# Performance work log

Measured on AMD Instinct MI355X. Metric: run time of the kernel, lower is better.

Reference implementation:

```python
import jax, jax.numpy as jnp
import numpy as np

NSIDE_SEND, NSIDE_REC = 128, 64
NPIX_SEND = 12 * NSIDE_SEND * NSIDE_SEND  # 196608 edges (one per fine pixel)
NPIX_REC = 12 * NSIDE_REC * NSIDE_REC     # 49152 coarse pixels
RATIO = NPIX_SEND // NPIX_REC             # 4 children per coarse pixel
B, F_IN = 2, 128
EMBED_OUT, LIN_OUT = 64, 128
LIN_IN = EMBED_OUT + F_IN


def setup_inputs() -> dict:
    key = jax.random.key(0)
    ks = jax.random.split(key, 9)
    s = 0.02
    # buffers (deterministic, from HEALPix nested ordering)
    edge_attr = (jnp.arange(NPIX_SEND, dtype=jnp.float32) % RATIO).reshape(-1, 1)
    edge_rec = (jnp.arange(NPIX_SEND, dtype=jnp.int32) // RATIO)
    return {
        "x": jax.random.normal(ks[0], (B, NPIX_SEND, F_IN), dtype=jnp.float32),
        "edge_attr": edge_attr,
        "edge_rec": edge_rec,
        # edge embedder MLP: 1 -> 64 -> 64
        "we1": jax.random.normal(ks[1], (1, EMBED_OUT), dtype=jnp.float32) * s,
        "be1": jnp.zeros((EMBED_OUT,), dtype=jnp.float32),
        "we2": jax.random.normal(ks[2], (EMBED_OUT, EMBED_OUT), dtype=jnp.float32) * s,
        "be2": jnp.zeros((EMBED_OUT,), dtype=jnp.float32),
        # final FeedForward: 192 -> 128 -> 128
        "wf1": jax.random.normal(ks[3], (LIN_IN, LIN_OUT), dtype=jnp.float32) * s,
        "bf1": jnp.zeros((LIN_OUT,), dtype=jnp.float32),
        "wf2": jax.random.normal(ks[4], (LIN_OUT, LIN_OUT), dtype=jnp.float32) * s,
        "bf2": jnp.zeros((LIN_OUT,), dtype=jnp.float32),
    }


def reference(x, edge_attr, edge_rec, we1, be1, we2, be2, wf1, bf1, wf2, bf2):
    # edge embedding MLP over the per-edge scalar attribute  [E, embed_out]
    e = jax.nn.gelu(edge_attr @ we1 + be1) @ we2 + be2
    # broadcast over batch and concat with node features  [B, E, lin_in]
    vm = jnp.concatenate([jnp.broadcast_to(e[None], (x.shape[0],) + e.shape), x], axis=-1)
    # scatter_sum over receiver pixels along the edge axis  [B, R, lin_in]
    agg = jax.vmap(lambda v: jax.ops.segment_sum(v, edge_rec, num_segments=NPIX_REC))(vm)
    # final FeedForward
    return jax.nn.gelu(agg @ wf1 + bf1) @ wf2 + bf2
```

## Files before the change

kernel.cpp:

```cpp
#include <hip/hip_runtime.h>


#define NPIX_REC  49152
#define F_IN      128
#define MTOT      98304
#define BM        64
#define NBLOCKS   (MTOT / BM)

#define LDS_C 0
#define LDS_G 512
#define LDS_E 768
#define LDS_X 1024
#define LDS_W 17408
#define LDS_TOT 50176

typedef __attribute__((ext_vector_type(4))) float f32x4;
typedef __attribute__((ext_vector_type(8))) short bf16x8;

__device__ __forceinline__ float gelu_tanh(float v) {
  float u = 0.7978845608028654f * (v + 0.044715f * v * v * v);
  float e = __expf(2.0f * u);
  return 0.5f * v * (1.0f + (1.0f - 2.0f / (e + 1.0f)));
}

__device__ __forceinline__ unsigned int f2bf(float f) {
  unsigned int u = __builtin_bit_cast(unsigned int, f);
  u += 0x7FFFu + ((u >> 16) & 1u);
  return u >> 16;
}

__device__ __forceinline__ void rawbar() {
  asm volatile("s_waitcnt lgkmcnt(0)" ::: "memory");
  __builtin_amdgcn_s_barrier();
  __builtin_amdgcn_sched_barrier(0);
}

__global__ __launch_bounds__(256, 3) void heal_all(
    const float* __restrict__ x,
    const float* __restrict__ we1, const float* __restrict__ be1,
    const float* __restrict__ we2, const float* __restrict__ be2,
    const float* __restrict__ wf1, const float* __restrict__ bf1,
    const float* __restrict__ wf2, const float* __restrict__ bf2,
    float* __restrict__ out) {
  __shared__ unsigned char smem[LDS_TOT];
  const int t = threadIdx.x;
  const int w = t >> 6, l = t & 63;
  const int cr = l & 15, kg = l >> 4;

  const int gr0 = blockIdx.x * BM;
  const float* xb = x + (size_t)gr0 * 512;

  const int pk = t >> 4, pn = t & 15;
  f32x4 w1v[8][2];
  #pragma unroll
  for (int rr = 0; rr < 8; ++rr) {
    const f32x4* p = (const f32x4*)(wf1 + (size_t)(64 + pk * 8 + rr) * 128 + pn * 8);
    w1v[rr][0] = p[0]; w1v[rr][1] = p[1];
  }

  float b2v[8];
  #pragma unroll
  for (int f = 0; f < 8; ++f) b2v[f] = bf2[f * 16 + cr];

  {
    const int kq = l & 31;
    const int rh = l >> 5;
    #pragma unroll 4
    for (int it = 0; it < 8; ++it) {
      int m = w * 16 + it * 2 + rh;
      const f32x4* rp = (const f32x4*)(xb + (size_t)(4 * m) * F_IN) + kq;
      f32x4 s = (rp[0] + rp[32]) + (rp[64] + rp[96]);
      uint2 val;
      val.x = f2bf(s.x) | (f2bf(s.y) << 16);
      val.y = f2bf(s.z) | (f2bf(s.w) << 16);
      unsigned int byte = (unsigned int)(m * 256 + kq * 8) ^ (unsigned int)((m & 7) << 4);
      *(uint2*)(smem + LDS_X + byte) = val;
    }
  }

  if (t < 64) {
    float wv = we1[t], bv = be1[t];
    float g = 0.f;
    #pragma unroll
    for (int a = 0; a < 4; ++a) g += gelu_tanh((float)a * wv + bv);
    ((float*)(smem + LDS_G))[t] = g;
  }
  rawbar();
  if (t < 64) {
    float s = 4.0f * be2[t];
    const float* G = (const float*)(smem + LDS_G);
    #pragma unroll 8
    for (int h = 0; h < 64; ++h) s += G[h] * we2[h * 64 + t];
    ((float*)(smem + LDS_E))[t] = s;
  }
  rawbar();
  if (t < 128) {
    float s = bf1[t];
    const float* E = (const float*)(smem + LDS_E);
    #pragma unroll 8
    for (int i = 0; i < 64; ++i) s += E[i] * wf1[(size_t)i * 128 + t];
    ((float*)(smem + LDS_C))[t] = s;
  }

  #pragma unroll
  for (int j = 0; j < 8; ++j) {
    float e0 = (j < 4) ? w1v[0][0][j] : w1v[0][1][j - 4];
    float e1 = (j < 4) ? w1v[1][0][j] : w1v[1][1][j - 4];
    float e2 = (j < 4) ? w1v[2][0][j] : w1v[2][1][j - 4];
    float e3 = (j < 4) ? w1v[3][0][j] : w1v[3][1][j - 4];
    float e4 = (j < 4) ? w1v[4][0][j] : w1v[4][1][j - 4];
    float e5 = (j < 4) ? w1v[5][0][j] : w1v[5][1][j - 4];
    float e6 = (j < 4) ? w1v[6][0][j] : w1v[6][1][j - 4];
    float e7 = (j < 4) ? w1v[7][0][j] : w1v[7][1][j - 4];
    uint4 o;
    o.x = f2bf(e0) | (f2bf(e1) << 16);
    o.y = f2bf(e2) | (f2bf(e3) << 16);
    o.z = f2bf(e4) | (f2bf(e5) << 16);
    o.w = f2bf(e6) | (f2bf(e7) << 16);
    int n = pn * 8 + j;
    unsigned int byte = (unsigned int)(n * 256) + (unsigned int)((pk ^ j) << 4);
    *(uint4*)(smem + LDS_W + byte) = o;
  }

  uint4 o2[8];
  {
    f32x4 w2v[8][2];
    #pragma unroll
    for (int rr = 0; rr < 8; ++rr) {
      const f32x4* p = (const f32x4*)(wf2 + (size_t)(pk * 8 + rr) * 128 + pn * 8);
      w2v[rr][0] = p[0]; w2v[rr][1] = p[1];
    }
    #pragma unroll
    for (int j = 0; j < 8; ++j) {
      float e0 = (j < 4) ? w2v[0][0][j] : w2v[0][1][j - 4];
      float e1 = (j < 4) ? w2v[1][0][j] : w2v[1][1][j - 4];
      float e2 = (j < 4) ? w2v[2][0][j] : w2v[2][1][j - 4];
      float e3 = (j < 4) ? w2v[3][0][j] : w2v[3][1][j - 4];
      float e4 = (j < 4) ? w2v[4][0][j] : w2v[4][1][j - 4];
      float e5 = (j < 4) ? w2v[5][0][j] : w2v[5][1][j - 4];
      float e6 = (j < 4) ? w2v[6][0][j] : w2v[6][1][j - 4];
      float e7 = (j < 4) ? w2v[7][0][j] : w2v[7][1][j - 4];
      o2[j].x = f2bf(e0) | (f2bf(e1) << 16);
      o2[j].y = f2bf(e2) | (f2bf(e3) << 16);
      o2[j].z = f2bf(e4) | (f2bf(e5) << 16);
      o2[j].w = f2bf(e6) | (f2bf(e7) << 16);
    }
  }

  __syncthreads();

  const int arow = w * 16 + cr;
  const unsigned int aswz = (unsigned int)((arow & 7) << 4);
  const unsigned int abase = (unsigned int)(arow * 256 + kg * 16);
  const unsigned int bswz = (unsigned int)((cr & 7) << 4);

  bf16x8 a[4];
  #pragma unroll
  for (int kk = 0; kk < 4; ++kk)
    a[kk] = *(const bf16x8*)(smem + LDS_X + ((abase + kk * 64) ^ aswz));

  float c1v[8];
  {
    const float* c1 = (const float*)(smem + LDS_C);
    #pragma unroll
    for (int f = 0; f < 8; ++f) c1v[f] = c1[f * 16 + cr];
  }

  f32x4 acc[8];
  #pragma unroll
  for (int f = 0; f < 8; ++f) {
    f32x4 z = {0.f, 0.f, 0.f, 0.f};
    acc[f] = z;
    unsigned int nbase = (unsigned int)((f * 16 + cr) * 256 + kg * 16);
    #pragma unroll
    for (int kk = 0; kk < 4; ++kk) {
      bf16x8 bfrag = *(const bf16x8*)(smem + LDS_W + ((nbase + kk * 64) ^ bswz));
      acc[f] = __builtin_amdgcn_mfma_f32_16x16x32_bf16(a[kk], bfrag, acc[f], 0, 0, 0);
    }
  }

  #pragma unroll
  for (int f = 0; f < 8; ++f) {
    #pragma unroll
    for (int q = 0; q < 4; ++q) {
      float v = gelu_tanh(acc[f][q] + c1v[f]);
      int hrow = w * 16 + kg * 4 + q;
      unsigned int byte = (unsigned int)(hrow * 256 + (f * 16 + cr) * 2)
                        ^ (unsigned int)((hrow & 7) << 4);
      *(unsigned short*)(smem + LDS_X + byte) = (unsigned short)f2bf(v);
    }
  }

  __syncthreads();

  bf16x8 a2[4];
  #pragma unroll
  for (int kk = 0; kk < 4; ++kk)
    a2[kk] = *(const bf16x8*)(smem + LDS_X + ((abase + kk * 64) ^ aswz));

  #pragma unroll
  for (int j = 0; j < 8; ++j) {
    int n = pn * 8 + j;
    unsigned int byte = (unsigned int)(n * 256) + (unsigned int)((pk ^ j) << 4);
    *(uint4*)(smem + LDS_W + byte) = o2[j];
  }
  __syncthreads();

  f32x4 acc2[8];
  #pragma unroll
  for (int f = 0; f < 8; ++f) {
    f32x4 z = {0.f, 0.f, 0.f, 0.f};
    acc2[f] = z;
    unsigned int nbase = (unsigned int)((f * 16 + cr) * 256 + kg * 16);
    #pragma unroll
    for (int kk = 0; kk < 4; ++kk) {
      bf16x8 bfrag = *(const bf16x8*)(smem + LDS_W + ((nbase + kk * 64) ^ bswz));
      acc2[f] = __builtin_amdgcn_mfma_f32_16x16x32_bf16(a2[kk], bfrag, acc2[f], 0, 0, 0);
    }
  }

  #pragma unroll
  for (int q = 0; q < 4; ++q) {
    int orow = gr0 + w * 16 + kg * 4 + q;
    float* op = out + (size_t)orow * 128;
    #pragma unroll
    for (int f = 0; f < 8; ++f)
      op[f * 16 + cr] = acc2[f][q] + b2v[f];
  }
}

extern "C" void kernel_launch(void* const* d_in, const int* in_sizes, int n_in,
                              void* d_out, int out_size, void* d_ws, size_t ws_size,
                              hipStream_t stream) {
  const float* x   = (const float*)d_in[0];
  const float* we1 = (const float*)d_in[3];
  const float* be1 = (const float*)d_in[4];
  const float* we2 = (const float*)d_in[5];
  const float* be2 = (const float*)d_in[6];
  const float* wf1 = (const float*)d_in[7];
  const float* bf1 = (const float*)d_in[8];
  const float* wf2 = (const float*)d_in[9];
  const float* bf2 = (const float*)d_in[10];
  float* out = (float*)d_out;

  hipLaunchKernelGGL(heal_all, dim3(NBLOCKS), dim3(256), 0, stream,
                     x, we1, be1, we2, be2, wf1, bf1, wf2, bf2, out);
}
```

Baseline: 71.09 us.

## Double rows per block and split weight staging across thread halves

Doubles the block to 512 threads and 128 output rows, so the per-block setup (bias vector, edge-embedding constant, bf16 conversion of both weight matrices) is shared across twice as many rows. The first 256 threads stage the wf1 x-part and the second 256 stage wf2, instead of every thread converting both. Adds an extra XOR term to the LDS swizzle of the weight tiles to spread bank accesses. In exchange, LDS per block grows to about 66 KB, which limits blocks per CU, and the grid has half as many blocks.

New measurement: 70.56 us. No clear change (-0.7%).

```diff
diff --git a/kernel.cpp b/kernel.cpp
--- a/kernel.cpp
+++ b/kernel.cpp
@@ -4,15 +4,15 @@
 #define NPIX_REC  49152
 #define F_IN      128
 #define MTOT      98304
-#define BM        64
+#define BM        128
 #define NBLOCKS   (MTOT / BM)
 
 #define LDS_C 0
 #define LDS_G 512
 #define LDS_E 768
 #define LDS_X 1024
-#define LDS_W 17408
-#define LDS_TOT 50176
+#define LDS_W 33792
+#define LDS_TOT 66560
 
 typedef __attribute__((ext_vector_type(4))) float f32x4;
 typedef __attribute__((ext_vector_type(8))) short bf16x8;
@@ -35,7 +35,7 @@
   __builtin_amdgcn_sched_barrier(0);
 }
 
-__global__ __launch_bounds__(256, 3) void heal_all(
+__global__ __launch_bounds__(512, 4) void heal_all(
     const float* __restrict__ x,
     const float* __restrict__ we1, const float* __restrict__ be1,
     const float* __restrict__ we2, const float* __restrict__ be2,
@@ -50,12 +50,14 @@
   const int gr0 = blockIdx.x * BM;
   const float* xb = x + (size_t)gr0 * 512;
 
-  const int pk = t >> 4, pn = t & 15;
-  f32x4 w1v[8][2];
+  const int tt = t & 255;
+  const int pk = tt >> 4, pn = tt & 15;
+  const float* wsrc = (t < 256) ? (wf1 + (size_t)64 * 128) : wf2;
+  f32x4 wv[8][2];
   #pragma unroll
   for (int rr = 0; rr < 8; ++rr) {
-    const f32x4* p = (const f32x4*)(wf1 + (size_t)(64 + pk * 8 + rr) * 128 + pn * 8);
-    w1v[rr][0] = p[0]; w1v[rr][1] = p[1];
+    const f32x4* p = (const f32x4*)(wsrc + (size_t)(pk * 8 + rr) * 128 + pn * 8);
+    wv[rr][0] = p[0]; wv[rr][1] = p[1];
   }
 
   float b2v[8];
@@ -79,10 +81,10 @@
   }
 
   if (t < 64) {
-    float wv = we1[t], bv = be1[t];
+    float wvv = we1[t], bv = be1[t];
     float g = 0.f;
     #pragma unroll
-    for (int a = 0; a < 4; ++a) g += gelu_tanh((float)a * wv + bv);
+    for (int a = 0; a < 4; ++a) g += gelu_tanh((float)a * wvv + bv);
     ((float*)(smem + LDS_G))[t] = g;
   }
   rawbar();
@@ -102,48 +104,28 @@
     ((float*)(smem + LDS_C))[t] = s;
   }
 
+  uint4 o2[8];
   #pragma unroll
   for (int j = 0; j < 8; ++j) {
-    float e0 = (j < 4) ? w1v[0][0][j] : w1v[0][1][j - 4];
-    float e1 = (j < 4) ? w1v[1][0][j] : w1v[1][1][j - 4];
-    float e2 = (j < 4) ? w1v[2][0][j] : w1v[2][1][j - 4];
-    float e3 = (j < 4) ? w1v[3][0][j] : w1v[3][1][j - 4];
-    float e4 = (j < 4) ? w1v[4][0][j] : w1v[4][1][j - 4];
-    float e5 = (j < 4) ? w1v[5][0][j] : w1v[5][1][j - 4];
-    float e6 = (j < 4) ? w1v[6][0][j] : w1v[6][1][j - 4];
-    float e7 = (j < 4) ? w1v[7][0][j] : w1v[7][1][j - 4];
+    float e0 = (j < 4) ? wv[0][0][j] : wv[0][1][j - 4];
+    float e1 = (j < 4) ? wv[1][0][j] : wv[1][1][j - 4];
+    float e2 = (j < 4) ? wv[2][0][j] : wv[2][1][j - 4];
+    float e3 = (j < 4) ? wv[3][0][j] : wv[3][1][j - 4];
+    float e4 = (j < 4) ? wv[4][0][j] : wv[4][1][j - 4];
+    float e5 = (j < 4) ? wv[5][0][j] : wv[5][1][j - 4];
+    float e6 = (j < 4) ? wv[6][0][j] : wv[6][1][j - 4];
+    float e7 = (j < 4) ? wv[7][0][j] : wv[7][1][j - 4];
     uint4 o;
     o.x = f2bf(e0) | (f2bf(e1) << 16);
     o.y = f2bf(e2) | (f2bf(e3) << 16);
     o.z = f2bf(e4) | (f2bf(e5) << 16);
     o.w = f2bf(e6) | (f2bf(e7) << 16);
-    int n = pn * 8 + j;
-    unsigned int byte = (unsigned int)(n * 256) + (unsigned int)((pk ^ j) << 4);
-    *(uint4*)(smem + LDS_W + byte) = o;
-  }
-
-  uint4 o2[8];
-  {
-    f32x4 w2v[8][2];
-    #pragma unroll
-    for (int rr = 0; rr < 8; ++rr) {
-      const f32x4* p = (const f32x4*)(wf2 + (size_t)(pk * 8 + rr) * 128 + pn * 8);
-      w2v[rr][0] = p[0]; w2v[rr][1] = p[1];
-    }
-    #pragma unroll
-    for (int j = 0; j < 8; ++j) {
-      float e0 = (j < 4) ? w2v[0][0][j] : w2v[0][1][j - 4];
-      float e1 = (j < 4) ? w2v[1][0][j] : w2v[1][1][j - 4];
-      float e2 = (j < 4) ? w2v[2][0][j] : w2v[2][1][j - 4];
-      float e3 = (j < 4) ? w2v[3][0][j] : w2v[3][1][j - 4];
-      float e4 = (j < 4) ? w2v[4][0][j] : w2v[4][1][j - 4];
-      float e5 = (j < 4) ? w2v[5][0][j] : w2v[5][1][j - 4];
-      float e6 = (j < 4) ? w2v[6][0][j] : w2v[6][1][j - 4];
-      float e7 = (j < 4) ? w2v[7][0][j] : w2v[7][1][j - 4];
-      o2[j].x = f2bf(e0) | (f2bf(e1) << 16);
-      o2[j].y = f2bf(e2) | (f2bf(e3) << 16);
-      o2[j].z = f2bf(e4) | (f2bf(e5) << 16);
-      o2[j].w = f2bf(e6) | (f2bf(e7) << 16);
+    if (t < 256) {
+      int n = pn * 8 + j;
+      unsigned int byte = (unsigned int)(n * 256) + (unsigned int)((pk ^ j ^ (pn & 7)) << 4);
+      *(uint4*)(smem + LDS_W + byte) = o;
+    } else {
+      o2[j] = o;
     }
   }
 
@@ -152,7 +134,6 @@
   const int arow = w * 16 + cr;
   const unsigned int aswz = (unsigned int)((arow & 7) << 4);
   const unsigned int abase = (unsigned int)(arow * 256 + kg * 16);
-  const unsigned int bswz = (unsigned int)((cr & 7) << 4);
 
   bf16x8 a[4];
   #pragma unroll
@@ -171,10 +152,12 @@
   for (int f = 0; f < 8; ++f) {
     f32x4 z = {0.f, 0.f, 0.f, 0.f};
     acc[f] = z;
-    unsigned int nbase = (unsigned int)((f * 16 + cr) * 256 + kg * 16);
+    int n = f * 16 + cr;
+    unsigned int g = (unsigned int)(((n & 7) ^ ((n >> 3) & 7)) << 4);
+    unsigned int nbase = (unsigned int)(n * 256 + kg * 16);
     #pragma unroll
     for (int kk = 0; kk < 4; ++kk) {
-      bf16x8 bfrag = *(const bf16x8*)(smem + LDS_W + ((nbase + kk * 64) ^ bswz));
+      bf16x8 bfrag = *(const bf16x8*)(smem + LDS_W + ((nbase + kk * 64) ^ g));
       acc[f] = __builtin_amdgcn_mfma_f32_16x16x32_bf16(a[kk], bfrag, acc[f], 0, 0, 0);
     }
   }
@@ -198,11 +181,13 @@
   for (int kk = 0; kk < 4; ++kk)
     a2[kk] = *(const bf16x8*)(smem + LDS_X + ((abase + kk * 64) ^ aswz));
 
-  #pragma unroll
-  for (int j = 0; j < 8; ++j) {
-    int n = pn * 8 + j;
-    unsigned int byte = (unsigned int)(n * 256) + (unsigned int)((pk ^ j) << 4);
-    *(uint4*)(smem + LDS_W + byte) = o2[j];
+  if (t >= 256) {
+    #pragma unroll
+    for (int j = 0; j < 8; ++j) {
+      int n = pn * 8 + j;
+      unsigned int byte = (unsigned int)(n * 256) + (unsigned int)((pk ^ j ^ (pn & 7)) << 4);
+      *(uint4*)(smem + LDS_W + byte) = o2[j];
+    }
   }
   __syncthreads();
 
@@ -211,10 +196,12 @@
   for (int f = 0; f < 8; ++f) {
     f32x4 z = {0.f, 0.f, 0.f, 0.f};
     acc2[f] = z;
-    unsigned int nbase = (unsigned int)((f * 16 + cr) * 256 + kg * 16);
+    int n = f * 16 + cr;
+    unsigned int g = (unsigned int)(((n & 7) ^ ((n >> 3) & 7)) << 4);
+    unsigned int nbase = (unsigned int)(n * 256 + kg * 16);
     #pragma unroll
     for (int kk = 0; kk < 4; ++kk) {
-      bf16x8 bfrag = *(const bf16x8*)(smem + LDS_W + ((nbase + kk * 64) ^ bswz));
+      bf16x8 bfrag = *(const bf16x8*)(smem + LDS_W + ((nbase + kk * 64) ^ g));
       acc2[f] = __builtin_amdgcn_mfma_f32_16x16x32_bf16(a2[kk], bfrag, acc2[f], 0, 0, 0);
     }
   }
@@ -243,6 +230,6 @@
   const float* bf2 = (const float*)d_in[10];
   float* out = (float*)d_out;
 
-  hipLaunchKernelGGL(heal_all, dim3(NBLOCKS), dim3(256), 0, stream,
+  hipLaunchKernelGGL(heal_all, dim3(NBLOCKS), dim3(512), 0, stream,
                      x, we1, be1, we2, be2, wf1, bf1, wf2, bf2, out);
 }
```
